# Kernel optimization log

Measured on AMD Instinct MI355X. Metric: run time of the kernel, lower is better.

## Reference

```python
import jax, jax.numpy as jnp
import numpy as np

NA, NQ, FDIM, NC, HID = 512, 4096, 2, 16, 64
CUTOFF = 6.0
GAMMA = 10.0
BOX = 12.0


def setup_inputs() -> dict:
    key = jax.random.key(0)
    ks = jax.random.split(key, 16)
    s = lambda k, shp, fan: jax.random.normal(k, shp, jnp.float32) * (1.0 / np.sqrt(fan))
    return {
        "atom_pos": jax.random.uniform(ks[0], (NA, 3), jnp.float32) * BOX,
        "atom_feat": jax.random.normal(ks[1], (NA, FDIM), jnp.float32),
        "query_pos": jax.random.uniform(ks[2], (NQ, 3), jnp.float32) * BOX,
        "W1": s(ks[3], (FDIM + NC, HID), FDIM + NC), "b1": jnp.zeros((HID,), jnp.float32),
        "W2": s(ks[4], (HID, HID), HID), "b2": jnp.zeros((HID,), jnp.float32),
        "W3": s(ks[5], (HID, HID // 2), HID), "b3": jnp.zeros((HID // 2,), jnp.float32),
        "W4": s(ks[6], (HID // 2, 1), HID // 2), "b4": jnp.zeros((1,), jnp.float32),
        "W5": s(ks[7], (3, 64), 3), "b5": jnp.zeros((64,), jnp.float32),
        "W6": s(ks[8], (64, 3), 64), "b6": jnp.zeros((3,), jnp.float32),
    }


def _forward(atom_pos, atom_feat, query_pos, W1, b1, W2, b2, W3, b3, W4, b4, W5, b5, W6, b6):
    centers = jnp.linspace(0.0, CUTOFF, NC, dtype=jnp.float32)  # RBF centers
    rel = query_pos[:, None, :] - atom_pos[None, :, :]          # (Nq,Na,3)
    dist = jnp.linalg.norm(rel + 1e-12, axis=-1)                 # (Nq,Na) (matches torch.norm(rel+eps))
    mask = (dist <= CUTOFF).astype(dist.dtype)
    rbf = jnp.exp(-GAMMA * (dist[..., None] - centers) ** 2)     # (Nq,Na,Nc)
    feat_b = jnp.broadcast_to(atom_feat[None], (query_pos.shape[0],) + atom_feat.shape)
    atom_input = jnp.concatenate([feat_b, rbf], axis=-1)         # (Nq,Na,F+Nc)
    h = jax.nn.relu(atom_input @ W1 + b1)
    h = jax.nn.relu(h @ W2 + b2)                                 # (Nq,Na,H)
    scalar_w = (jax.nn.relu(h @ W3 + b3) @ W4 + b4)[..., 0] * mask  # (Nq,Na)
    dir_vec = rel / (dist[..., None] + 1e-12)                    # (Nq,Na,3)
    weighted = jnp.einsum('qa,qad->qd', scalar_w, dir_vec)       # (Nq,3)
    out = jax.nn.relu(weighted @ W5 + b5) @ W6 + b6              # (Nq,3)
    return out


def reference(atom_pos, atom_feat, query_pos, W1, b1, W2, b2, W3, b3, W4, b4, W5, b5, W6, b6):
    return _forward(atom_pos, atom_feat, query_pos, W1, b1, W2, b2, W3, b3, W4, b4, W5, b5, W6, b6)
```

## Files before the change

kernel.cpp:

```cpp
#include <hip/hip_runtime.h>
#include <math.h>


typedef _Float16 f16x4 __attribute__((ext_vector_type(4)));
typedef _Float16 f16x2 __attribute__((ext_vector_type(2)));
typedef float    f32x4 __attribute__((ext_vector_type(4)));

#define CAP 352
#define NT  2

#define MFMA16(A,B,C) __builtin_amdgcn_mfma_f32_16x16x16f16(A,B,C,0,0,0)

__device__ __forceinline__ float exp2_fast(float x) {
    float r;
    asm("v_exp_f32 %0, %1" : "=v"(r) : "v"(x));
    return r;
}

__device__ __forceinline__ f16x4 relu_cvt(f32x4 c) {
    return f16x4{(_Float16)fmaxf(c[0],0.f), (_Float16)fmaxf(c[1],0.f),
                 (_Float16)fmaxf(c[2],0.f), (_Float16)fmaxf(c[3],0.f)};
}

__global__ __launch_bounds__(64) void repack_kernel(
    const float* __restrict__ W1, const float* __restrict__ b1,
    const float* __restrict__ W2, const float* __restrict__ b2,
    const float* __restrict__ W3, const float* __restrict__ b3,
    const float* __restrict__ W4, char* __restrict__ ws)
{
    const int b = blockIdx.x, l = threadIdx.x;
    const int col = l & 15, quad = l >> 4;
    if (b < 32) {
        f16x4 v;
        #pragma unroll
        for (int j = 0; j < 4; ++j) {
            float x;
            if (b < 8) {
                const int kc = b >> 2, mt = b & 3;
                const int k = kc*16 + quad*4 + j;
                if (k < 16)       x = W1[(k+2)*64 + mt*16 + col];
                else if (k == 16) x = W1[        mt*16 + col];
                else if (k == 17) x = W1[ 64   + mt*16 + col];
                else if (k == 18) x = b1[        mt*16 + col];
                else              x = 0.0f;
            } else if (b < 24) {
                const int idx = b - 8, kc = idx >> 2, mt = idx & 3;
                const int k = kc*16 + quad*4 + j;
                x = W2[k*64 + mt*16 + col];
            } else {
                const int idx = b - 24, kc = idx >> 1, mt = idx & 1;
                const int k = kc*16 + quad*4 + j;
                x = W3[k*32 + mt*16 + col];
            }
            v[j] = (_Float16)x;
        }
        *(f16x4*)(ws + (b*64 + l)*8) = v;
    } else {
        const int d = b - 32;
        float o[4];
        #pragma unroll
        for (int rr = 0; rr < 4; ++rr) {
            const int idx = quad*4 + rr;
            if (d < 4)      o[rr] = b2[d*16 + idx];
            else if (d < 6) o[rr] = b3[(d-4)*16 + idx];
            else            o[rr] = W4[(d-6)*16 + idx];
        }
        *(float4*)(ws + 16384 + (d*64 + l)*16) = make_float4(o[0],o[1],o[2],o[3]);
    }
}

__global__ __launch_bounds__(256, 3) void aqfn_kernel(
    const float* __restrict__ atom_pos,
    const float* __restrict__ atom_feat,
    const float* __restrict__ query_pos,
    const float* __restrict__ b4,
    const float* __restrict__ W5, const float* __restrict__ b5,
    const float* __restrict__ W6, const float* __restrict__ b6,
    const char*  __restrict__ ws,
    float* __restrict__ out)
{
    __shared__ __align__(16) float4 rbufs[4][CAP];
    __shared__ __align__(8)  f16x2  fbufs[4][CAP];
    __shared__ __align__(16) f16x4  wlds[2048];

    const int tid  = threadIdx.x;
    const int wave = __builtin_amdgcn_readfirstlane(tid >> 6);
    const int lane = tid & 63;
    const int col  = lane & 15;
    const int quad = lane >> 4;
    const int q    = blockIdx.x * 4 + wave;

    float4* rb = rbufs[wave];
    f16x2*  fb = fbufs[wave];

    {
        const f16x4* wsrc = (const f16x4*)ws;
        #pragma unroll
        for (int i = 0; i < 8; ++i)
            wlds[tid + i*256] = wsrc[tid + i*256];
    }

    const float4* wsb = (const float4*)(ws + 16384);
    float4 b2v[4], b3v[2], w4v[2];
    #pragma unroll
    for (int mt = 0; mt < 4; ++mt) b2v[mt] = wsb[mt*64 + lane];
    #pragma unroll
    for (int mt = 0; mt < 2; ++mt) { b3v[mt] = wsb[(4+mt)*64 + lane];
                                     w4v[mt] = wsb[(6+mt)*64 + lane]; }
    const float b4v = b4[0];

    const float w5x = W5[lane], w5y = W5[64+lane], w5z = W5[128+lane];
    const float b5v = b5[lane];
    const float w6x = W6[lane*3+0], w6y = W6[lane*3+1], w6z = W6[lane*3+2];

    const float qx = query_pos[q*3+0];
    const float qy = query_pos[q*3+1];
    const float qz = query_pos[q*3+2];

    int off = 0;
    #pragma unroll
    for (int it = 0; it < 8; ++it) {
        const int a = it*64 + lane;
        const float rx = qx - atom_pos[a*3+0];
        const float ry = qy - atom_pos[a*3+1];
        const float rz = qz - atom_pos[a*3+2];
        const float f0 = atom_feat[a*2+0];
        const float f1 = atom_feat[a*2+1];
        const float ex = __fadd_rn(rx, 1e-12f);
        const float ey = __fadd_rn(ry, 1e-12f);
        const float ez = __fadd_rn(rz, 1e-12f);
        const float dd = __fadd_rn(__fadd_rn(__fmul_rn(ex,ex), __fmul_rn(ey,ey)),
                                   __fmul_rn(ez,ez));
        const float dist = sqrtf(dd);
        const unsigned long long m = __ballot(dist <= 6.0f);
        const int p = off + (int)__popcll(m & ((1ull << lane) - 1ull));
        if (((m >> lane) & 1ull) && p < CAP) {
            rb[p] = make_float4(rx, ry, rz, dist);
            fb[p] = f16x2{(_Float16)f0, (_Float16)f1};
        }
        off += (int)__popcll(m);
    }
    const int count = off > CAP ? CAP : off;

    __syncthreads();

    float wacc0 = 0.f, wacc1 = 0.f, wacc2 = 0.f;
    const int nchunks = (count + (NT*16 - 1)) / (NT*16);
    const float cbase = 1.5193132f * (float)(quad*4);

    #pragma unroll 1
    for (int chunk = 0; chunk < nchunks; ++chunk) {
        const int row0 = chunk * (NT*16);

        int wb = 0;
        asm volatile("" : "+v"(wb));

        float4 rv[NT]; f16x2 ffv[NT];
        #pragma unroll
        for (int u = 0; u < NT; ++u) {
            int pr = row0 + u*16 + col;
            if (pr >= count) pr = count - 1;
            rv[u]  = rb[pr];
            ffv[u] = fb[pr];
        }

        f16x4 xa0[NT], xa1[NT];
        #pragma unroll
        for (int u = 0; u < NT; ++u) {
            const float base = __fmul_rn(rv[u].w, 3.7982831f) - cbase;
            #pragma unroll
            for (int j = 0; j < 4; ++j) {
                const float t = base - 1.5193132f * (float)j;
                xa0[u][j] = (_Float16)exp2_fast(t * -t);
            }
            const bool q0 = (quad == 0);
            xa1[u] = f16x4{q0 ? ffv[u][0] : (_Float16)0.f,
                           q0 ? ffv[u][1] : (_Float16)0.f,
                           (_Float16)(q0 ? 1.f : 0.f),
                           (_Float16)0.f};
        }

        f16x4 t1[2][4];
        #pragma unroll
        for (int kc = 0; kc < 2; ++kc)
            #pragma unroll
            for (int mt = 0; mt < 4; ++mt)
                t1[kc][mt] = wlds[wb + (kc*4 + mt)*64 + lane];
        f16x4 a2[NT][4];
        #pragma unroll
        for (int u = 0; u < NT; ++u)
            #pragma unroll
            for (int mt = 0; mt < 4; ++mt) {
                f32x4 c = {0.f, 0.f, 0.f, 0.f};
                c = MFMA16(t1[0][mt], xa0[u], c);
                c = MFMA16(t1[1][mt], xa1[u], c);
                a2[u][mt] = relu_cvt(c);
            }

        f16x4 t2[4][4];
        #pragma unroll
        for (int kc = 0; kc < 4; ++kc)
            #pragma unroll
            for (int mt = 0; mt < 4; ++mt)
                t2[kc][mt] = wlds[wb + (8 + kc*4 + mt)*64 + lane];
        f16x4 a3[NT][4];
        #pragma unroll
        for (int u = 0; u < NT; ++u)
            #pragma unroll
            for (int mt = 0; mt < 4; ++mt) {
                f32x4 c = {b2v[mt].x, b2v[mt].y, b2v[mt].z, b2v[mt].w};
                #pragma unroll
                for (int kc = 0; kc < 4; ++kc)
                    c = MFMA16(t2[kc][mt], a2[u][kc], c);
                a3[u][mt] = relu_cvt(c);
            }

        f16x4 t3[4][2];
        #pragma unroll
        for (int kc = 0; kc < 4; ++kc)
            #pragma unroll
            for (int mt = 0; mt < 2; ++mt)
                t3[kc][mt] = wlds[wb + (24 + kc*2 + mt)*64 + lane];
        #pragma unroll
        for (int u = 0; u < NT; ++u) {
            float s = 0.f;
            #pragma unroll
            for (int mt = 0; mt < 2; ++mt) {
                f32x4 c = {b3v[mt].x, b3v[mt].y, b3v[mt].z, b3v[mt].w};
                #pragma unroll
                for (int kc = 0; kc < 4; ++kc)
                    c = MFMA16(t3[kc][mt], a3[u][kc], c);
                const float* wv = &w4v[mt].x;
                #pragma unroll
                for (int rr = 0; rr < 4; ++rr)
                    s = fmaf(fmaxf(c[rr], 0.f), wv[rr], s);
            }
            s += __shfl_xor(s, 16);
            s += __shfl_xor(s, 32);
            s += b4v;
            const int   p2  = row0 + u*16 + col;
            const float inv = __builtin_amdgcn_rcpf(rv[u].w + 1e-12f);
            const float wm  = (p2 < count) ? (s * inv) : 0.f;
            wacc0 = fmaf(wm, rv[u].x, wacc0);
            wacc1 = fmaf(wm, rv[u].y, wacc1);
            wacc2 = fmaf(wm, rv[u].z, wacc2);
        }
    }

    #pragma unroll
    for (int o = 1; o < 64; o <<= 1) {
        wacc0 += __shfl_xor(wacc0, o);
        wacc1 += __shfl_xor(wacc1, o);
        wacc2 += __shfl_xor(wacc2, o);
    }
    const float v0 = wacc0 * 0.25f;
    const float v1 = wacc1 * 0.25f;
    const float v2 = wacc2 * 0.25f;

    float th = fmaf(v0, w5x, fmaf(v1, w5y, fmaf(v2, w5z, b5v)));
    th = fmaxf(th, 0.f);
    float o0 = th * w6x, o1 = th * w6y, o2 = th * w6z;
    #pragma unroll
    for (int o = 1; o < 64; o <<= 1) {
        o0 += __shfl_xor(o0, o);
        o1 += __shfl_xor(o1, o);
        o2 += __shfl_xor(o2, o);
    }
    if (lane == 0) {
        out[q*3+0] = o0 + b6[0];
        out[q*3+1] = o1 + b6[1];
        out[q*3+2] = o2 + b6[2];
    }
}

extern "C" void kernel_launch(void* const* d_in, const int* in_sizes, int n_in,
                              void* d_out, int out_size, void* d_ws, size_t ws_size,
                              hipStream_t stream) {
    const float* atom_pos  = (const float*)d_in[0];
    const float* atom_feat = (const float*)d_in[1];
    const float* query_pos = (const float*)d_in[2];
    const float* W1 = (const float*)d_in[3];  const float* b1 = (const float*)d_in[4];
    const float* W2 = (const float*)d_in[5];  const float* b2 = (const float*)d_in[6];
    const float* W3 = (const float*)d_in[7];  const float* b3 = (const float*)d_in[8];
    const float* W4 = (const float*)d_in[9];  const float* b4 = (const float*)d_in[10];
    const float* W5 = (const float*)d_in[11]; const float* b5 = (const float*)d_in[12];
    const float* W6 = (const float*)d_in[13]; const float* b6 = (const float*)d_in[14];
    float* out = (float*)d_out;
    char*  ws  = (char*)d_ws;

    hipLaunchKernelGGL(repack_kernel, dim3(40), dim3(64), 0, stream,
                       W1, b1, W2, b2, W3, b3, W4, ws);
    hipLaunchKernelGGL(aqfn_kernel, dim3(1024), dim3(256), 0, stream,
                       atom_pos, atom_feat, query_pos, b4, W5, b5, W6, b6,
                       (const char*)ws, out);
}
```

Measured before the change: 113.8 us.

## Cut registers and LDS to raise occupancy to four blocks per CU

Raises the launch bound from 3 to 4 blocks per CU. To make room, it stops keeping bias and W4 values in registers for the whole kernel and instead stages them in LDS, re-reading them per chunk. Atom features are packed as f16x2 into the w slot of the float4 buffer, which removes the separate feature buffer, and distance is recomputed from rx/ry/rz in the chunk loop. The W5/W6 loads are delayed to the epilogue. The cost is extra per-chunk LDS reads and sqrt work in exchange for lower register and LDS pressure.

```diff
diff --git a/kernel.cpp b/kernel.cpp
--- a/kernel.cpp
+++ b/kernel.cpp
@@ -20,6 +20,11 @@
 __device__ __forceinline__ f16x4 relu_cvt(f32x4 c) {
     return f16x4{(_Float16)fmaxf(c[0],0.f), (_Float16)fmaxf(c[1],0.f),
                  (_Float16)fmaxf(c[2],0.f), (_Float16)fmaxf(c[3],0.f)};
+}
+
+__device__ __forceinline__ float pack_f16x2(float a, float b) {
+    f16x2 h{(_Float16)a, (_Float16)b};
+    return __builtin_bit_cast(float, h);
 }
 
 __global__ __launch_bounds__(64) void repack_kernel(
@@ -56,20 +61,19 @@
         }
         *(f16x4*)(ws + (b*64 + l)*8) = v;
     } else {
-        const int d = b - 32;
-        float o[4];
-        #pragma unroll
-        for (int rr = 0; rr < 4; ++rr) {
-            const int idx = quad*4 + rr;
-            if (d < 4)      o[rr] = b2[d*16 + idx];
-            else if (d < 6) o[rr] = b3[(d-4)*16 + idx];
-            else            o[rr] = W4[(d-6)*16 + idx];
-        }
-        *(float4*)(ws + 16384 + (d*64 + l)*16) = make_float4(o[0],o[1],o[2],o[3]);
-    }
-}
-
-__global__ __launch_bounds__(256, 3) void aqfn_kernel(
+        float* bo = (float*)(ws + 16384);
+        #pragma unroll
+        for (int i = l; i < 128; i += 64) {
+            float x;
+            if (i < 64)       x = b2[i];
+            else if (i < 96)  x = b3[i - 64];
+            else              x = W4[i - 96];
+            bo[i] = x;
+        }
+    }
+}
+
+__global__ __launch_bounds__(256, 4) void aqfn_kernel(
     const float* __restrict__ atom_pos,
     const float* __restrict__ atom_feat,
     const float* __restrict__ query_pos,
@@ -80,8 +84,8 @@
     float* __restrict__ out)
 {
     __shared__ __align__(16) float4 rbufs[4][CAP];
-    __shared__ __align__(8)  f16x2  fbufs[4][CAP];
     __shared__ __align__(16) f16x4  wlds[2048];
+    __shared__ __align__(16) float  biaslds[128];
 
     const int tid  = threadIdx.x;
     const int wave = __builtin_amdgcn_readfirstlane(tid >> 6);
@@ -91,27 +95,16 @@
     const int q    = blockIdx.x * 4 + wave;
 
     float4* rb = rbufs[wave];
-    f16x2*  fb = fbufs[wave];
 
     {
         const f16x4* wsrc = (const f16x4*)ws;
         #pragma unroll
         for (int i = 0; i < 8; ++i)
             wlds[tid + i*256] = wsrc[tid + i*256];
-    }
-
-    const float4* wsb = (const float4*)(ws + 16384);
-    float4 b2v[4], b3v[2], w4v[2];
-    #pragma unroll
-    for (int mt = 0; mt < 4; ++mt) b2v[mt] = wsb[mt*64 + lane];
-    #pragma unroll
-    for (int mt = 0; mt < 2; ++mt) { b3v[mt] = wsb[(4+mt)*64 + lane];
-                                     w4v[mt] = wsb[(6+mt)*64 + lane]; }
+        if (tid < 128) biaslds[tid] = ((const float*)(ws + 16384))[tid];
+    }
+
     const float b4v = b4[0];
-
-    const float w5x = W5[lane], w5y = W5[64+lane], w5z = W5[128+lane];
-    const float b5v = b5[lane];
-    const float w6x = W6[lane*3+0], w6y = W6[lane*3+1], w6z = W6[lane*3+2];
 
     const float qx = query_pos[q*3+0];
     const float qy = query_pos[q*3+1];
@@ -134,10 +127,8 @@
         const float dist = sqrtf(dd);
         const unsigned long long m = __ballot(dist <= 6.0f);
         const int p = off + (int)__popcll(m & ((1ull << lane) - 1ull));
-        if (((m >> lane) & 1ull) && p < CAP) {
-            rb[p] = make_float4(rx, ry, rz, dist);
-            fb[p] = f16x2{(_Float16)f0, (_Float16)f1};
-        }
+        if (((m >> lane) & 1ull) && p < CAP)
+            rb[p] = make_float4(rx, ry, rz, pack_f16x2(f0, f1));
         off += (int)__popcll(m);
     }
     const int count = off > CAP ? CAP : off;
@@ -154,20 +145,30 @@
 
         int wb = 0;
         asm volatile("" : "+v"(wb));
-
-        float4 rv[NT]; f16x2 ffv[NT];
+        const float4* bias4 = (const float4*)biaslds;
+
+        float4 rv[NT]; float dvv[NT]; f16x2 ffv[NT];
         #pragma unroll
         for (int u = 0; u < NT; ++u) {
             int pr = row0 + u*16 + col;
             if (pr >= count) pr = count - 1;
-            rv[u]  = rb[pr];
-            ffv[u] = fb[pr];
+            rv[u] = rb[pr];
+        }
+        #pragma unroll
+        for (int u = 0; u < NT; ++u) {
+            ffv[u] = __builtin_bit_cast(f16x2, rv[u].w);
+            const float ex = __fadd_rn(rv[u].x, 1e-12f);
+            const float ey = __fadd_rn(rv[u].y, 1e-12f);
+            const float ez = __fadd_rn(rv[u].z, 1e-12f);
+            const float dd = __fadd_rn(__fadd_rn(__fmul_rn(ex,ex), __fmul_rn(ey,ey)),
+                                       __fmul_rn(ez,ez));
+            dvv[u] = sqrtf(dd);
         }
 
         f16x4 xa0[NT], xa1[NT];
         #pragma unroll
         for (int u = 0; u < NT; ++u) {
-            const float base = __fmul_rn(rv[u].w, 3.7982831f) - cbase;
+            const float base = __fmul_rn(dvv[u], 3.7982831f) - cbase;
             #pragma unroll
             for (int j = 0; j < 4; ++j) {
                 const float t = base - 1.5193132f * (float)j;
@@ -203,6 +204,9 @@
             #pragma unroll
             for (int mt = 0; mt < 4; ++mt)
                 t2[kc][mt] = wlds[wb + (8 + kc*4 + mt)*64 + lane];
+        float4 b2v[4];
+        #pragma unroll
+        for (int mt = 0; mt < 4; ++mt) b2v[mt] = bias4[wb + mt*4 + quad];
         f16x4 a3[NT][4];
         #pragma unroll
         for (int u = 0; u < NT; ++u)
@@ -221,6 +225,12 @@
             #pragma unroll
             for (int mt = 0; mt < 2; ++mt)
                 t3[kc][mt] = wlds[wb + (24 + kc*2 + mt)*64 + lane];
+        float4 b3v[2], w4v[2];
+        #pragma unroll
+        for (int mt = 0; mt < 2; ++mt) {
+            b3v[mt] = bias4[wb + 16 + mt*4 + quad];
+            w4v[mt] = bias4[wb + 24 + mt*4 + quad];
+        }
         #pragma unroll
         for (int u = 0; u < NT; ++u) {
             float s = 0.f;
@@ -239,7 +249,7 @@
             s += __shfl_xor(s, 32);
             s += b4v;
             const int   p2  = row0 + u*16 + col;
-            const float inv = __builtin_amdgcn_rcpf(rv[u].w + 1e-12f);
+            const float inv = __builtin_amdgcn_rcpf(dvv[u] + 1e-12f);
             const float wm  = (p2 < count) ? (s * inv) : 0.f;
             wacc0 = fmaf(wm, rv[u].x, wacc0);
             wacc1 = fmaf(wm, rv[u].y, wacc1);
@@ -257,9 +267,17 @@
     const float v1 = wacc1 * 0.25f;
     const float v2 = wacc2 * 0.25f;
 
+    int hz = 0;
+    asm volatile("" : "+v"(hz));
+    const float w5x = W5[hz + lane];
+    const float w5y = W5[hz + 64 + lane];
+    const float w5z = W5[hz + 128 + lane];
+    const float b5v = b5[hz + lane];
     float th = fmaf(v0, w5x, fmaf(v1, w5y, fmaf(v2, w5z, b5v)));
     th = fmaxf(th, 0.f);
-    float o0 = th * w6x, o1 = th * w6y, o2 = th * w6z;
+    float o0 = th * W6[hz + lane*3+0];
+    float o1 = th * W6[hz + lane*3+1];
+    float o2 = th * W6[hz + lane*3+2];
     #pragma unroll
     for (int o = 1; o < 64; o <<= 1) {
         o0 += __shfl_xor(o0, o);
@@ -288,7 +306,7 @@
     float* out = (float*)d_out;
     char*  ws  = (char*)d_ws;
 
-    hipLaunchKernelGGL(repack_kernel, dim3(40), dim3(64), 0, stream,
+    hipLaunchKernelGGL(repack_kernel, dim3(33), dim3(64), 0, stream,
                        W1, b1, W2, b2, W3, b3, W4, ws);
     hipLaunchKernelGGL(aqfn_kernel, dim3(1024), dim3(256), 0, stream,
                        atom_pos, atom_feat, query_pos, b4, W5, b5, W6, b6,
```

Result: no change. 112.3 us (-1.3%).
